# Performance work log

Hardware: AMD Instinct MI355X
Metric: run time of the kernel (lower is better)

## Reference

```python
import jax, jax.numpy as jnp
import numpy as np

ETA = 0.01
EPSILON = 1e-08


def setup_inputs() -> dict:
    key = jax.random.key(0)
    k1, k2 = jax.random.split(key)
    B, N = 2000000, 16  # batch (time steps), num_assets
    weights = jax.random.uniform(k1, (B, N), dtype=jnp.float32)
    next_returns = jax.random.normal(k2, (B, N), dtype=jnp.float32) * 0.02
    return {"weights": weights, "next_returns": next_returns}


def reference(weights, next_returns):
    # portfolio return per time step: (B,)
    R = jnp.sum(weights * next_returns, axis=1)
    batch_size = R.shape[0]
    eta = jnp.asarray(ETA, R.dtype)
    eps = jnp.asarray(EPSILON, R.dtype)

    def step(carry, R_t):
        A_prev, B_prev = carry
        delta_A = eta * (R_t - A_prev)
        delta_B = eta * (R_t * R_t - B_prev)
        variance = jnp.maximum(B_prev - A_prev * A_prev, eps)
        denom = variance ** 1.5
        D_t = (B_prev * delta_A - 0.5 * A_prev * delta_B) / denom
        return (A_prev + delta_A, B_prev + delta_B), D_t

    init = (jnp.asarray(0.0, R.dtype), jnp.asarray(EPSILON, R.dtype))
    _, D = jax.lax.scan(step, init, R)
    return -jnp.sum(D) / batch_size
```

## Files before the change

kernel.cpp:

```cpp
#include <hip/hip_runtime.h>


#define D_ETA 0.01
#define D_C   (1.0 - D_ETA)
#define D_EPS 1e-8

constexpr int BLOCK   = 256;
constexpr int CHUNK1  = 1024;
constexpr int LPT1    = CHUNK1 / BLOCK;
constexpr int PASSES  = CHUNK1 / 64;
constexpr int CHUNK4  = 2048;
constexpr int LPT4    = CHUNK4 / BLOCK;

typedef float f32x4 __attribute__((ext_vector_type(4)));

__device__ __forceinline__ void block_scan(double& m, double& sA, double& sB,
                                           double* mS, double* aS, double* bS) {
    int tid = threadIdx.x;
    mS[tid] = m; aS[tid] = sA; bS[tid] = sB;
    __syncthreads();
#pragma unroll
    for (int off = 1; off < BLOCK; off <<= 1) {
        double pm = 1.0, pa = 0.0, pb = 0.0;
        if (tid >= off) { pm = mS[tid - off]; pa = aS[tid - off]; pb = bS[tid - off]; }
        __syncthreads();
        if (tid >= off) {
            sA = m * pa + sA;
            sB = m * pb + sB;
            m  = pm * m;
        }
        mS[tid] = m; aS[tid] = sA; bS[tid] = sB;
        __syncthreads();
    }
}

__global__ __launch_bounds__(BLOCK, 6) void k1_fused(
    const float* __restrict__ w, const float* __restrict__ x, int nrows,
    float* __restrict__ Rws,
    double* __restrict__ blkM, double* __restrict__ blkA, double* __restrict__ blkB)
{
    __shared__ double Qs[2][CHUNK1];
    __shared__ double mS[BLOCK], aS[BLOCK], bS[BLOCK];

    const int tid = threadIdx.x;
    const int b   = blockIdx.x;
    const long long base = (long long)b * CHUNK1;
    const int q    = tid & 3;
    const int rsub = tid >> 2;
    const f32x4* w4 = (const f32x4*)w;
    const f32x4* x4 = (const f32x4*)x;

    const bool full = (base + CHUNK1 <= (long long)nrows);

    if (full) {
        const long long f0 = base * 4 + tid;
        f32x4 a0 = __builtin_nontemporal_load(&w4[f0]);
        f32x4 c0 = __builtin_nontemporal_load(&x4[f0]);
        f32x4 a1 = __builtin_nontemporal_load(&w4[f0 + 256]);
        f32x4 c1 = __builtin_nontemporal_load(&x4[f0 + 256]);
        f32x4 a2 = __builtin_nontemporal_load(&w4[f0 + 512]);
        f32x4 c2 = __builtin_nontemporal_load(&x4[f0 + 512]);
        f32x4 a3 = __builtin_nontemporal_load(&w4[f0 + 768]);
        f32x4 c3 = __builtin_nontemporal_load(&x4[f0 + 768]);
#pragma unroll
        for (int p = 0; p < PASSES; ++p) {
            f32x4 an = (f32x4)(0.f);
            f32x4 cn = (f32x4)(0.f);
            if (p + 4 < PASSES) {
                an = __builtin_nontemporal_load(&w4[f0 + (long long)(p + 4) * 256]);
                cn = __builtin_nontemporal_load(&x4[f0 + (long long)(p + 4) * 256]);
            }
            __builtin_amdgcn_sched_barrier(0);
            double d = (double)a0.x * c0.x + (double)a0.y * c0.y
                     + (double)a0.z * c0.z + (double)a0.w * c0.w;
            d += __shfl_xor(d, 1, 64);
            if ((q & 1) == 0)
                Qs[q >> 1][p * 64 + rsub] = d;
            a0 = a1; c0 = c1;
            a1 = a2; c1 = c2;
            a2 = a3; c2 = c3;
            a3 = an; c3 = cn;
        }
    } else {
        for (int p = 0; p < PASSES; ++p) {
            long long row = base + (long long)p * 64 + rsub;
            double d = 0.0;
            if (row < (long long)nrows) {
                long long f = row * 4 + q;
                f32x4 a = w4[f], c = x4[f];
                d = (double)a.x * c.x + (double)a.y * c.y
                  + (double)a.z * c.z + (double)a.w * c.w;
            }
            d += __shfl_xor(d, 1, 64);
            if ((q & 1) == 0 && row < (long long)nrows)
                Qs[q >> 1][p * 64 + rsub] = d;
        }
    }
    __syncthreads();

    long long g0 = base + (long long)tid * LPT1;
    long long rem = (long long)nrows - g0;
    int len = rem >= LPT1 ? LPT1 : (rem > 0 ? (int)rem : 0);

    float rv[LPT1];
#pragma unroll
    for (int r = 0; r < LPT1; ++r) {
        int lr = tid * LPT1 + r;
        rv[r] = (float)(Qs[0][lr] + Qs[1][lr]);
    }

    if (len == LPT1) {
        *(float4*)(Rws + g0) = make_float4(rv[0], rv[1], rv[2], rv[3]);
    } else {
        for (int k = 0; k < len; ++k) Rws[g0 + k] = rv[k];
    }

    double m = 1.0, sA = 0.0, sB = 0.0;
    for (int k = 0; k < len; ++k) {
        double r = (double)rv[k];
        sA = D_C * sA + D_ETA * r;
        sB = D_C * sB + D_ETA * (r * r);
        m *= D_C;
    }
    block_scan(m, sA, sB, mS, aS, bS);
    if (tid == BLOCK - 1) {
        blkM[b] = m;
        blkA[b] = sA;
        blkB[b] = sB;
    }
}

__device__ __forceinline__ float row_R(const float* __restrict__ w,
                                       const float* __restrict__ x,
                                       long long row) {
    const float4* w4 = (const float4*)(w + row * 16);
    const float4* x4 = (const float4*)(x + row * 16);
    double d0, d1, d2, d3;
    {
        float4 a = w4[0], b = x4[0];
        d0 = (double)a.x * b.x + (double)a.y * b.y
           + (double)a.z * b.z + (double)a.w * b.w;
    }
    {
        float4 a = w4[1], b = x4[1];
        d1 = (double)a.x * b.x + (double)a.y * b.y
           + (double)a.z * b.z + (double)a.w * b.w;
    }
    {
        float4 a = w4[2], b = x4[2];
        d2 = (double)a.x * b.x + (double)a.y * b.y
           + (double)a.z * b.z + (double)a.w * b.w;
    }
    {
        float4 a = w4[3], b = x4[3];
        d3 = (double)a.x * b.x + (double)a.y * b.y
           + (double)a.z * b.z + (double)a.w * b.w;
    }
    return (float)((d0 + d1) + (d2 + d3));
}

__global__ __launch_bounds__(BLOCK) void k2_partials(
    const float* __restrict__ w, const float* __restrict__ x, int nrows,
    double* __restrict__ blkM, double* __restrict__ blkA, double* __restrict__ blkB)
{
    __shared__ double mS[BLOCK], aS[BLOCK], bS[BLOCK];
    int tid = threadIdx.x;
    long long g0 = (long long)blockIdx.x * CHUNK1 + (long long)tid * LPT1;
    long long rem = (long long)nrows - g0;
    int len = rem >= LPT1 ? LPT1 : (rem > 0 ? (int)rem : 0);

    double m = 1.0, sA = 0.0, sB = 0.0;
    for (int k = 0; k < len; ++k) {
        double r = (double)row_R(w, x, g0 + k);
        sA = D_C * sA + D_ETA * r;
        sB = D_C * sB + D_ETA * (r * r);
        m *= D_C;
    }
    block_scan(m, sA, sB, mS, aS, bS);
    if (tid == BLOCK - 1) {
        blkM[blockIdx.x] = m;
        blkA[blockIdx.x] = sA;
        blkB[blockIdx.x] = sB;
    }
}

__global__ __launch_bounds__(BLOCK) void k4_dsum(
    const float* __restrict__ Rws,
    const float* __restrict__ w, const float* __restrict__ x, int nrows,
    const double* __restrict__ blkM, const double* __restrict__ blkA,
    const double* __restrict__ blkB,
    double* __restrict__ bsum)
{
    __shared__ double mS[BLOCK], aS[BLOCK], bS[BLOCK];
    __shared__ double wsum[BLOCK / 64];
    const int tid = threadIdx.x;
    const int b   = blockIdx.x;

    double Astart, Bstart;
    {
        const int H = 2 * b;
        const int K = (H + BLOCK - 1) / BLOCK;
        double cm = 1.0, ca = 0.0, cb = 0.0;
        int s0 = tid * K;
        int s1 = s0 + K; if (s1 > H) s1 = H;
        for (int g = s0; g < s1; ++g) {
            double mg = blkM[g], ag = blkA[g], bg = blkB[g];
            ca = mg * ca + ag;
            cb = mg * cb + bg;
            cm *= mg;
        }
        block_scan(cm, ca, cb, mS, aS, bS);
        double M  = mS[BLOCK - 1];
        double SA = aS[BLOCK - 1];
        double SB = bS[BLOCK - 1];
        Astart = SA;
        Bstart = M * D_EPS + SB;
    }
    __syncthreads();

    long long g0 = (long long)b * CHUNK4 + (long long)tid * LPT4;
    long long rem = (long long)nrows - g0;
    int len = rem >= LPT4 ? LPT4 : (rem > 0 ? (int)rem : 0);

    float rv[LPT4];
    if (Rws) {
        if (len == LPT4) {
            f32x4 u = __builtin_nontemporal_load((const f32x4*)(Rws + g0));
            f32x4 v = __builtin_nontemporal_load((const f32x4*)(Rws + g0 + 4));
            rv[0]=u.x; rv[1]=u.y; rv[2]=u.z; rv[3]=u.w;
            rv[4]=v.x; rv[5]=v.y; rv[6]=v.z; rv[7]=v.w;
        } else {
            for (int k = 0; k < len; ++k) rv[k] = Rws[g0 + k];
        }
    } else {
        for (int k = 0; k < len; ++k) rv[k] = row_R(w, x, g0 + k);
    }

    double m = 1.0, sA = 0.0, sB = 0.0;
    for (int k = 0; k < len; ++k) {
        double r = (double)rv[k];
        sA = D_C * sA + D_ETA * r;
        sB = D_C * sB + D_ETA * (r * r);
        m *= D_C;
    }
    block_scan(m, sA, sB, mS, aS, bS);

    double em = 1.0, ea = 0.0, eb = 0.0;
    if (tid > 0) { em = mS[tid - 1]; ea = aS[tid - 1]; eb = bS[tid - 1]; }
    double A = em * Astart + ea;
    double B = em * Bstart + eb;

    double dsum = 0.0;
    for (int k = 0; k < len; ++k) {
        double r = (double)rv[k];
        double dA = D_ETA * (r - A);
        double dB = D_ETA * (r * r - B);
        double var = B - A * A;
        if (var < D_EPS) var = D_EPS;
        double denom = var * sqrt(var);
        dsum += (B * dA - 0.5 * A * dB) / denom;
        A += dA;
        B += dB;
    }

#pragma unroll
    for (int off = 32; off > 0; off >>= 1) dsum += __shfl_down(dsum, off, 64);
    if ((tid & 63) == 0) wsum[tid >> 6] = dsum;
    __syncthreads();
    if (tid == 0) bsum[b] = wsum[0] + wsum[1] + wsum[2] + wsum[3];
}

__global__ __launch_bounds__(BLOCK) void k5_final(
    const double* __restrict__ bsum, int nb, int nrows, float* __restrict__ out)
{
    __shared__ double sh[BLOCK / 64];
    int tid = threadIdx.x;
    double s = 0.0;
    for (int i = tid; i < nb; i += BLOCK) s += bsum[i];
#pragma unroll
    for (int off = 32; off > 0; off >>= 1) s += __shfl_down(s, off, 64);
    if ((tid & 63) == 0) sh[tid >> 6] = s;
    __syncthreads();
    if (tid == 0) out[0] = (float)(-(sh[0] + sh[1] + sh[2] + sh[3]) / (double)nrows);
}

extern "C" void kernel_launch(void* const* d_in, const int* in_sizes, int n_in,
                              void* d_out, int out_size, void* d_ws, size_t ws_size,
                              hipStream_t stream)
{
    const float* w = (const float*)d_in[0];
    const float* x = (const float*)d_in[1];
    int nrows = in_sizes[0] / 16;
    int nb1 = (nrows + CHUNK1 - 1) / CHUNK1;
    int nb4 = (nrows + CHUNK4 - 1) / CHUNK4;

    char* ws = (char*)d_ws;
    double* blkM = (double*)(ws + 64);
    double* blkA = blkM + nb1;
    double* blkB = blkA + nb1;
    double* bsum = blkB + nb1;

    size_t off = 64 + ((size_t)3 * nb1 + nb4) * sizeof(double);
    off = (off + 255) & ~(size_t)255;
    float* Rws = nullptr;
    if (ws_size >= off + (size_t)nrows * sizeof(float))
        Rws = (float*)(ws + off);

    if (Rws) {
        k1_fused<<<nb1, BLOCK, 0, stream>>>(w, x, nrows, Rws, blkM, blkA, blkB);
    } else {
        k2_partials<<<nb1, BLOCK, 0, stream>>>(w, x, nrows, blkM, blkA, blkB);
    }
    k4_dsum<<<nb4, BLOCK, 0, stream>>>(Rws, w, x, nrows, blkM, blkA, blkB, bsum);
    k5_final<<<1, BLOCK, 0, stream>>>(bsum, nb4, nrows, (float*)d_out);
}
```

Measured before the change: 259.5 us.

## Fuse scan passes into single kernel with decoupled lookback via flags

Replaces the three-kernel pipeline (partials with an R workspace write, a second pass re-reading R, and a final reduce) with one kernel. Each block publishes its aggregate with a release flag, then spin-waits on all predecessor flags to compute its prefix, and the last-finishing block does the final reduction via an atomic counter. This removes the R round-trip through memory and two kernel launches. In exchange, each block reads every predecessor aggregate (quadratic total reads across roughly 2000 blocks), relies on blocks being scheduled in order to avoid spin deadlock, and adds a flag-init launch.

```diff
diff --git a/kernel.cpp b/kernel.cpp
--- a/kernel.cpp
+++ b/kernel.cpp
@@ -5,14 +5,22 @@
 #define D_C   (1.0 - D_ETA)
 #define D_EPS 1e-8
 
-constexpr int BLOCK   = 256;
-constexpr int CHUNK1  = 1024;
-constexpr int LPT1    = CHUNK1 / BLOCK;
-constexpr int PASSES  = CHUNK1 / 64;
-constexpr int CHUNK4  = 2048;
-constexpr int LPT4    = CHUNK4 / BLOCK;
+constexpr int BLOCK  = 256;
+constexpr int CHUNK  = 1024;
+constexpr int LPT    = CHUNK / BLOCK;
+constexpr int PASSES = CHUNK / 64;
 
 typedef float f32x4 __attribute__((ext_vector_type(4)));
+
+__device__ __forceinline__ void pub_d(double* p, double v) {
+    __hip_atomic_store((unsigned long long*)p, __double_as_longlong(v),
+                       __ATOMIC_RELAXED, __HIP_MEMORY_SCOPE_AGENT);
+}
+__device__ __forceinline__ double rd_d(const double* p) {
+    return __longlong_as_double(
+        __hip_atomic_load((const unsigned long long*)p,
+                          __ATOMIC_RELAXED, __HIP_MEMORY_SCOPE_AGENT));
+}
 
 __device__ __forceinline__ void block_scan(double& m, double& sA, double& sB,
                                            double* mS, double* aS, double* bS) {
@@ -34,23 +42,31 @@
     }
 }
 
-__global__ __launch_bounds__(BLOCK, 6) void k1_fused(
-    const float* __restrict__ w, const float* __restrict__ x, int nrows,
-    float* __restrict__ Rws,
-    double* __restrict__ blkM, double* __restrict__ blkA, double* __restrict__ blkB)
+__global__ __launch_bounds__(BLOCK) void k_init(int* __restrict__ flags, int n) {
+    int i = blockIdx.x * BLOCK + threadIdx.x;
+    if (i < n) flags[i] = 0;
+}
+
+__global__ __launch_bounds__(BLOCK, 4) void k_all(
+    const float* __restrict__ w, const float* __restrict__ x, int nrows, int nb,
+    double* __restrict__ aggM, double* __restrict__ aggA, double* __restrict__ aggB,
+    int* __restrict__ flags, double* __restrict__ bsum, int* __restrict__ done,
+    float* __restrict__ out)
 {
-    __shared__ double Qs[2][CHUNK1];
+    __shared__ double Qs[2][CHUNK];
     __shared__ double mS[BLOCK], aS[BLOCK], bS[BLOCK];
+    __shared__ double wsum[BLOCK / 64];
+    __shared__ int amLast;
 
     const int tid = threadIdx.x;
     const int b   = blockIdx.x;
-    const long long base = (long long)b * CHUNK1;
+    const long long base = (long long)b * CHUNK;
     const int q    = tid & 3;
     const int rsub = tid >> 2;
     const f32x4* w4 = (const f32x4*)w;
     const f32x4* x4 = (const f32x4*)x;
 
-    const bool full = (base + CHUNK1 <= (long long)nrows);
+    const bool full = (base + CHUNK <= (long long)nrows);
 
     if (full) {
         const long long f0 = base * 4 + tid;
@@ -98,21 +114,15 @@
     }
     __syncthreads();
 
-    long long g0 = base + (long long)tid * LPT1;
+    long long g0 = base + (long long)tid * LPT;
     long long rem = (long long)nrows - g0;
-    int len = rem >= LPT1 ? LPT1 : (rem > 0 ? (int)rem : 0);
-
-    float rv[LPT1];
-#pragma unroll
-    for (int r = 0; r < LPT1; ++r) {
-        int lr = tid * LPT1 + r;
+    int len = rem >= LPT ? LPT : (rem > 0 ? (int)rem : 0);
+
+    float rv[LPT];
+#pragma unroll
+    for (int r = 0; r < LPT; ++r) {
+        int lr = tid * LPT + r;
         rv[r] = (float)(Qs[0][lr] + Qs[1][lr]);
-    }
-
-    if (len == LPT1) {
-        *(float4*)(Rws + g0) = make_float4(rv[0], rv[1], rv[2], rv[3]);
-    } else {
-        for (int k = 0; k < len; ++k) Rws[g0 + k] = rv[k];
     }
 
     double m = 1.0, sA = 0.0, sB = 0.0;
@@ -124,87 +134,27 @@
     }
     block_scan(m, sA, sB, mS, aS, bS);
     if (tid == BLOCK - 1) {
-        blkM[b] = m;
-        blkA[b] = sA;
-        blkB[b] = sB;
-    }
-}
-
-__device__ __forceinline__ float row_R(const float* __restrict__ w,
-                                       const float* __restrict__ x,
-                                       long long row) {
-    const float4* w4 = (const float4*)(w + row * 16);
-    const float4* x4 = (const float4*)(x + row * 16);
-    double d0, d1, d2, d3;
-    {
-        float4 a = w4[0], b = x4[0];
-        d0 = (double)a.x * b.x + (double)a.y * b.y
-           + (double)a.z * b.z + (double)a.w * b.w;
-    }
-    {
-        float4 a = w4[1], b = x4[1];
-        d1 = (double)a.x * b.x + (double)a.y * b.y
-           + (double)a.z * b.z + (double)a.w * b.w;
-    }
-    {
-        float4 a = w4[2], b = x4[2];
-        d2 = (double)a.x * b.x + (double)a.y * b.y
-           + (double)a.z * b.z + (double)a.w * b.w;
-    }
-    {
-        float4 a = w4[3], b = x4[3];
-        d3 = (double)a.x * b.x + (double)a.y * b.y
-           + (double)a.z * b.z + (double)a.w * b.w;
-    }
-    return (float)((d0 + d1) + (d2 + d3));
-}
-
-__global__ __launch_bounds__(BLOCK) void k2_partials(
-    const float* __restrict__ w, const float* __restrict__ x, int nrows,
-    double* __restrict__ blkM, double* __restrict__ blkA, double* __restrict__ blkB)
-{
-    __shared__ double mS[BLOCK], aS[BLOCK], bS[BLOCK];
-    int tid = threadIdx.x;
-    long long g0 = (long long)blockIdx.x * CHUNK1 + (long long)tid * LPT1;
-    long long rem = (long long)nrows - g0;
-    int len = rem >= LPT1 ? LPT1 : (rem > 0 ? (int)rem : 0);
-
-    double m = 1.0, sA = 0.0, sB = 0.0;
-    for (int k = 0; k < len; ++k) {
-        double r = (double)row_R(w, x, g0 + k);
-        sA = D_C * sA + D_ETA * r;
-        sB = D_C * sB + D_ETA * (r * r);
-        m *= D_C;
-    }
-    block_scan(m, sA, sB, mS, aS, bS);
-    if (tid == BLOCK - 1) {
-        blkM[blockIdx.x] = m;
-        blkA[blockIdx.x] = sA;
-        blkB[blockIdx.x] = sB;
-    }
-}
-
-__global__ __launch_bounds__(BLOCK) void k4_dsum(
-    const float* __restrict__ Rws,
-    const float* __restrict__ w, const float* __restrict__ x, int nrows,
-    const double* __restrict__ blkM, const double* __restrict__ blkA,
-    const double* __restrict__ blkB,
-    double* __restrict__ bsum)
-{
-    __shared__ double mS[BLOCK], aS[BLOCK], bS[BLOCK];
-    __shared__ double wsum[BLOCK / 64];
-    const int tid = threadIdx.x;
-    const int b   = blockIdx.x;
+        pub_d(&aggM[b], m);
+        pub_d(&aggA[b], sA);
+        pub_d(&aggB[b], sB);
+        __hip_atomic_store(&flags[b], 1, __ATOMIC_RELEASE, __HIP_MEMORY_SCOPE_AGENT);
+    }
+    double em = 1.0, ea = 0.0, eb = 0.0;
+    if (tid > 0) { em = mS[tid - 1]; ea = aS[tid - 1]; eb = bS[tid - 1]; }
+    __syncthreads();
 
     double Astart, Bstart;
     {
-        const int H = 2 * b;
+        const int H = b;
         const int K = (H + BLOCK - 1) / BLOCK;
         double cm = 1.0, ca = 0.0, cb = 0.0;
         int s0 = tid * K;
         int s1 = s0 + K; if (s1 > H) s1 = H;
         for (int g = s0; g < s1; ++g) {
-            double mg = blkM[g], ag = blkA[g], bg = blkB[g];
+            while (__hip_atomic_load(&flags[g], __ATOMIC_ACQUIRE,
+                                     __HIP_MEMORY_SCOPE_AGENT) == 0)
+                __builtin_amdgcn_s_sleep(2);
+            double mg = rd_d(&aggM[g]), ag = rd_d(&aggA[g]), bg = rd_d(&aggB[g]);
             ca = mg * ca + ag;
             cb = mg * cb + bg;
             cm *= mg;
@@ -216,37 +166,7 @@
         Astart = SA;
         Bstart = M * D_EPS + SB;
     }
-    __syncthreads();
-
-    long long g0 = (long long)b * CHUNK4 + (long long)tid * LPT4;
-    long long rem = (long long)nrows - g0;
-    int len = rem >= LPT4 ? LPT4 : (rem > 0 ? (int)rem : 0);
-
-    float rv[LPT4];
-    if (Rws) {
-        if (len == LPT4) {
-            f32x4 u = __builtin_nontemporal_load((const f32x4*)(Rws + g0));
-            f32x4 v = __builtin_nontemporal_load((const f32x4*)(Rws + g0 + 4));
-            rv[0]=u.x; rv[1]=u.y; rv[2]=u.z; rv[3]=u.w;
-            rv[4]=v.x; rv[5]=v.y; rv[6]=v.z; rv[7]=v.w;
-        } else {
-            for (int k = 0; k < len; ++k) rv[k] = Rws[g0 + k];
-        }
-    } else {
-        for (int k = 0; k < len; ++k) rv[k] = row_R(w, x, g0 + k);
-    }
-
-    double m = 1.0, sA = 0.0, sB = 0.0;
-    for (int k = 0; k < len; ++k) {
-        double r = (double)rv[k];
-        sA = D_C * sA + D_ETA * r;
-        sB = D_C * sB + D_ETA * (r * r);
-        m *= D_C;
-    }
-    block_scan(m, sA, sB, mS, aS, bS);
-
-    double em = 1.0, ea = 0.0, eb = 0.0;
-    if (tid > 0) { em = mS[tid - 1]; ea = aS[tid - 1]; eb = bS[tid - 1]; }
+
     double A = em * Astart + ea;
     double B = em * Bstart + eb;
 
@@ -262,26 +182,30 @@
         A += dA;
         B += dB;
     }
-
 #pragma unroll
     for (int off = 32; off > 0; off >>= 1) dsum += __shfl_down(dsum, off, 64);
     if ((tid & 63) == 0) wsum[tid >> 6] = dsum;
     __syncthreads();
-    if (tid == 0) bsum[b] = wsum[0] + wsum[1] + wsum[2] + wsum[3];
-}
-
-__global__ __launch_bounds__(BLOCK) void k5_final(
-    const double* __restrict__ bsum, int nb, int nrows, float* __restrict__ out)
-{
-    __shared__ double sh[BLOCK / 64];
-    int tid = threadIdx.x;
-    double s = 0.0;
-    for (int i = tid; i < nb; i += BLOCK) s += bsum[i];
-#pragma unroll
-    for (int off = 32; off > 0; off >>= 1) s += __shfl_down(s, off, 64);
-    if ((tid & 63) == 0) sh[tid >> 6] = s;
-    __syncthreads();
-    if (tid == 0) out[0] = (float)(-(sh[0] + sh[1] + sh[2] + sh[3]) / (double)nrows);
+    if (tid == 0) {
+        double tot = wsum[0] + wsum[1] + wsum[2] + wsum[3];
+        pub_d(&bsum[b], tot);
+        int prev = __hip_atomic_fetch_add(done, 1, __ATOMIC_ACQ_REL,
+                                          __HIP_MEMORY_SCOPE_AGENT);
+        amLast = (prev == nb - 1);
+    }
+    __syncthreads();
+
+    if (amLast) {
+        double s = 0.0;
+        for (int i = tid; i < nb; i += BLOCK) s += rd_d(&bsum[i]);
+#pragma unroll
+        for (int off = 32; off > 0; off >>= 1) s += __shfl_down(s, off, 64);
+        if ((tid & 63) == 0) wsum[tid >> 6] = s;
+        __syncthreads();
+        if (tid == 0)
+            out[0] = (float)(-(wsum[0] + wsum[1] + wsum[2] + wsum[3])
+                             / (double)nrows);
+    }
 }
 
 extern "C" void kernel_launch(void* const* d_in, const int* in_sizes, int n_in,
@@ -291,26 +215,22 @@
     const float* w = (const float*)d_in[0];
     const float* x = (const float*)d_in[1];
     int nrows = in_sizes[0] / 16;
-    int nb1 = (nrows + CHUNK1 - 1) / CHUNK1;
-    int nb4 = (nrows + CHUNK4 - 1) / CHUNK4;
+    int nb = (nrows + CHUNK - 1) / CHUNK;
 
     char* ws = (char*)d_ws;
-    double* blkM = (double*)(ws + 64);
-    double* blkA = blkM + nb1;
-    double* blkB = blkA + nb1;
-    double* bsum = blkB + nb1;
-
-    size_t off = 64 + ((size_t)3 * nb1 + nb4) * sizeof(double);
-    off = (off + 255) & ~(size_t)255;
-    float* Rws = nullptr;
-    if (ws_size >= off + (size_t)nrows * sizeof(float))
-        Rws = (float*)(ws + off);
-
-    if (Rws) {
-        k1_fused<<<nb1, BLOCK, 0, stream>>>(w, x, nrows, Rws, blkM, blkA, blkB);
-    } else {
-        k2_partials<<<nb1, BLOCK, 0, stream>>>(w, x, nrows, blkM, blkA, blkB);
-    }
-    k4_dsum<<<nb4, BLOCK, 0, stream>>>(Rws, w, x, nrows, blkM, blkA, blkB, bsum);
-    k5_final<<<1, BLOCK, 0, stream>>>(bsum, nb4, nrows, (float*)d_out);
-}
+    double* aggM = (double*)(ws + 64);
+    double* aggA = aggM + nb;
+    double* aggB = aggA + nb;
+    double* bsum = aggB + nb;
+    int*    flags = (int*)(bsum + nb);
+    int*    done  = flags + nb;
+
+    size_t need = 64 + (size_t)4 * nb * sizeof(double) + (size_t)(nb + 1) * sizeof(int);
+    if (ws_size < need) return;
+
+    int initBlocks = (nb + 1 + BLOCK - 1) / BLOCK;
+    k_init<<<initBlocks, BLOCK, 0, stream>>>(flags, nb + 1);
+    k_all<<<nb, BLOCK, 0, stream>>>(w, x, nrows, nb,
+                                    aggM, aggA, aggB, flags, bsum, done,
+                                    (float*)d_out);
+}
```

Result: slower. 642.9 us (+147.8%).
